# Optimization experiments

Hardware: AMD Instinct MI355X
Metric: run time of the kernel (lower is better)

The kernel has to match this reference:

```python
import jax, jax.numpy as jnp
import numpy as np
import math

B, T, D = 2, 4096, 1024
HD = D // 2                      # head_dim
DEPTH = 12
LAMBDA_INIT = 0.8 - 0.6 * math.exp(-0.3 * DEPTH)
SCALING = HD ** -0.5
EPS = 1e-5


def setup_inputs() -> dict:
    key = jax.random.key(0)
    ks = jax.random.split(key, 11)
    f32 = jnp.float32
    return {
        "q": jax.random.normal(ks[0], (B, T, D), f32),
        "k": jax.random.normal(ks[1], (B, T, D), f32),
        "v": jax.random.normal(ks[2], (B, T, D), f32),
        "Wq": jax.random.normal(ks[3], (D, D), f32) * 0.02,
        "Wk": jax.random.normal(ks[4], (HD, D), f32) * 0.02,
        "Wv": jax.random.normal(ks[5], (D, D), f32) * 0.02,
        "Wo": jax.random.normal(ks[6], (D, D), f32) * 0.02,
        "lambda_q1": jax.random.normal(ks[7], (HD,), f32) * 0.1,
        "lambda_k1": jax.random.normal(ks[8], (HD,), f32) * 0.1,
        "lambda_q2": jax.random.normal(ks[9], (HD,), f32) * 0.1,
        "lambda_k2": jax.random.normal(ks[10], (HD,), f32) * 0.1,
    }


def reference(q, k, v, Wq, Wk, Wv, Wo, lambda_q1, lambda_k1, lambda_q2, lambda_k2):
    b, t, d = q.shape
    s = k.shape[1]
    # projections (Linear with no bias: x @ W.T)
    qp = (q @ Wq.T).reshape(b, t, 2, HD).transpose(0, 2, 1, 3) * SCALING  # [b,2,t,hd]
    kp = k @ Wk.T                                                          # [b,s,hd] (shared by both score heads)
    # dual score maps + softmax over src
    scores = jnp.einsum("bhtd,bsd->bhts", qp, kp)                          # [b,2,t,s]
    scores = jax.nn.softmax(scores.astype(jnp.float32), axis=-1).astype(qp.dtype)
    # lambda-weighted subtraction
    lam1 = jnp.exp(jnp.sum(lambda_q1 * lambda_k1))
    lam2 = jnp.exp(jnp.sum(lambda_q2 * lambda_k2))
    lam = lam1 - lam2 + LAMBDA_INIT
    attn_w = scores[:, 0] - lam * scores[:, 1]                             # [b,t,s]
    # value matmul
    vp = v @ Wv.T                                                          # [b,s,d]
    attn = jnp.einsum("bts,bsd->btd", attn_w, vp)                          # [b,t,d]
    # RMSNorm over last dim (2*head_dim == d), no affine
    rms = jax.lax.rsqrt(jnp.mean(jnp.square(attn), axis=-1, keepdims=True) + EPS)
    attn = attn * rms * (1.0 - LAMBDA_INIT)
    return attn @ Wo.T
```

## Files before the change

kernel.cpp:

```cpp
#include <hip/hip_runtime.h>
#include <stdint.h>
#include <stddef.h>

#define T_   4096
#define BT_  8192
#define SCALING_F      0.04419417382415922f
#define LAMBDA_INIT_F  0.7836057665316212f
#define ONE_MINUS_LI_F 0.2163942334683788f

typedef __attribute__((ext_vector_type(8))) short short8;
typedef __attribute__((ext_vector_type(4))) short short4v;
typedef __attribute__((ext_vector_type(4))) float f32x4;

__device__ __forceinline__ short f2bf(float f){
  uint32_t u = __float_as_uint(f);
  uint32_t r = (u + 0x7fffu + ((u >> 16) & 1u)) >> 16;
  return (short)(uint16_t)r;
}

__device__ __forceinline__ f32x4 mfma16(short8 a, short8 b, f32x4 c){
  return __builtin_amdgcn_mfma_f32_16x16x32_bf16(a, b, c, 0, 0, 0);
}

__device__ __forceinline__ void stage16(short* lds, const short* g){
  __builtin_amdgcn_global_load_lds(
      (const __attribute__((address_space(1))) void*)g,
      (__attribute__((address_space(3))) void*)lds, 16, 0, 0);
}

__global__ void k_cvt(const float* __restrict__ in, short* __restrict__ out, int n4){
  int i  = blockIdx.x*blockDim.x + threadIdx.x;
  int st = gridDim.x*blockDim.x;
  for (; i < n4; i += st){
    float4 v = ((const float4*)in)[i];
    short4v o;
    o.x = f2bf(v.x); o.y = f2bf(v.y); o.z = f2bf(v.z); o.w = f2bf(v.w);
    ((short4v*)out)[i] = o;
  }
}

template<int EPI>
__global__ __launch_bounds__(256, 3) void k_gemm(const short* __restrict__ A,
                                                 const short* __restrict__ Bm,
                                                 void* __restrict__ Cp, int ldc){
  __shared__ short As[128*32];
  __shared__ short Bs[128*32];
  const int tid = threadIdx.x;
  const int w = tid >> 6, l = tid & 63;
  const int m0 = blockIdx.x * 128;
  const int n0 = blockIdx.y * 128;
  const int wr = w >> 1, wc = w & 1;

  f32x4 acc[4][4] = {};

  const short* gA = A  + (size_t)(m0 + w*32 + (l>>2))*1024 + (l&3)*8;
  const short* gB = Bm + (size_t)(n0 + w*32 + (l>>2))*1024 + (l&3)*8;

  for (int k0 = 0; k0 < 1024; k0 += 32){
    stage16(As + w*1024,       gA + k0);
    stage16(As + w*1024 + 512, gA + 16*1024 + k0);
    stage16(Bs + w*1024,       gB + k0);
    stage16(Bs + w*1024 + 512, gB + 16*1024 + k0);
    __syncthreads();
    short8 aF[4], bF[4];
    #pragma unroll
    for (int i = 0; i < 4; i++){
      aF[i] = *(const short8*)&As[(wr*64 + i*16 + (l&15))*32 + (l>>4)*8];
      bF[i] = *(const short8*)&Bs[(wc*64 + i*16 + (l&15))*32 + (l>>4)*8];
    }
    #pragma unroll
    for (int i = 0; i < 4; i++)
      #pragma unroll
      for (int j = 0; j < 4; j++)
        acc[i][j] = mfma16(aF[i], bF[j], acc[i][j]);
    __syncthreads();
  }

  #pragma unroll
  for (int i = 0; i < 4; i++){
    #pragma unroll
    for (int j = 0; j < 4; j++){
      const size_t r0 = (size_t)m0 + wr*64 + i*16 + (l>>4)*4;
      const size_t c  = (size_t)n0 + wc*64 + j*16 + (l&15);
      #pragma unroll
      for (int rg = 0; rg < 4; rg++){
        float v = acc[i][j][rg];
        if (EPI == 2){
          ((float*)Cp)[(r0+rg)*(size_t)ldc + c] = v;
        } else {
          if (EPI == 1) v *= SCALING_F;
          ((short*)Cp)[(r0+rg)*(size_t)ldc + c] = f2bf(v);
        }
      }
    }
  }
}

__global__ __launch_bounds__(512, 2) void k_attn(
    const short* __restrict__ QP, const short* __restrict__ KP,
    const short* __restrict__ VPT,
    const float* __restrict__ lq1, const float* __restrict__ lk1,
    const float* __restrict__ lq2, const float* __restrict__ lk2,
    short* __restrict__ Ab)
{
  __shared__ short Ks[2][64*512];
  __shared__ short Pl[2][32][72];
  __shared__ float lsum[8][16];
  __shared__ float rinv[2][32];
  __shared__ float ssq[8][32];

  int wg = blockIdx.x;
  wg = (wg & 7)*32 + (wg >> 3);
  const int b  = wg >> 7;
  const int t0 = (wg & 127) * 32;

  const int tid = threadIdx.x;
  const int w = tid >> 6, l = tid & 63;

  float s1 = 0.f, s2 = 0.f;
  #pragma unroll
  for (int i = 0; i < 8; i++){
    int idx = l*8 + i;
    s1 += lq1[idx]*lk1[idx];
    s2 += lq2[idx]*lk2[idx];
  }
  #pragma unroll
  for (int off = 1; off < 64; off <<= 1){
    s1 += __shfl_xor(s1, off, 64);
    s2 += __shfl_xor(s2, off, 64);
  }
  const float lam = __expf(s1) - __expf(s2) + LAMBDA_INIT_F;

  const int rc = w >> 1, h = rc >> 1, tch = rc & 1, scb = w & 1;
  short8 qF[16];
  {
    const short* qb = QP + (size_t)(b*T_ + t0 + tch*16 + (l&15))*1024 + h*512 + (l>>4)*8;
    #pragma unroll
    for (int kk = 0; kk < 16; kk++) qF[kk] = *(const short8*)(qb + kk*32);
  }

  f32x4 acc[4][8] = {};
  float lacc[4] = {0.f,0.f,0.f,0.f};

  const short* kpb = KP  + (size_t)(b*T_)*512;
  const short* vb  = VPT + (size_t)(w*128 + (l&15))*BT_ + b*T_ + (l>>4)*8;

  const int jx = (l >> 4) ^ (l & 3);
  const int kx = (l >> 2) & 1;
  const int row0 = (2*scb)*16 + (l & 15);

  {
    short* kdst = &Ks[0][w*8*512];
    const short* ksrc = kpb + (size_t)(w*8)*512;
    #pragma unroll
    for (int j = 0; j < 8; j++)
      stage16(kdst + j*512, ksrc + (size_t)j*512 + ((l ^ j)*8));
  }
  __syncthreads();

  for (int st = 0; st < 64; st++){
    const int s0  = st*64;
    const int cur = st & 1;

    f32x4 sa0 = {0.f,0.f,0.f,0.f}, sa1 = {0.f,0.f,0.f,0.f};
    {
      const short* p0 = &Ks[cur][0] + row0*512 + jx*8;
      const short* p1 = p0 + 16*512;
      #pragma unroll
      for (int kk = 0; kk < 16; kk++){
        short8 b0 = *(const short8*)(p0 + ((kk ^ kx) << 5));
        short8 b1 = *(const short8*)(p1 + ((kk ^ kx) << 5));
        sa0 = mfma16(qF[kk], b0, sa0);
        sa1 = mfma16(qF[kk], b1, sa1);
      }
    }

    if (st + 1 < 64){
      short* kdst = &Ks[cur ^ 1][w*8*512];
      const short* ksrc = kpb + (size_t)((st+1)*64 + w*8)*512;
      #pragma unroll
      for (int j = 0; j < 8; j++)
        stage16(kdst + j*512, ksrc + (size_t)j*512 + ((l ^ j)*8));
    }

    #pragma unroll
    for (int rg = 0; rg < 4; rg++){
      float e0 = __expf(sa0[rg]);
      float e1 = __expf(sa1[rg]);
      lacc[rg] += e0 + e1;
      int row = tch*16 + (l>>4)*4 + rg;
      Pl[h][row][(2*scb+0)*16 + (l&15)] = f2bf(e0);
      Pl[h][row][(2*scb+1)*16 + (l&15)] = f2bf(e1);
    }

    asm volatile("s_waitcnt lgkmcnt(0)" ::: "memory");
    __builtin_amdgcn_s_barrier();

    #pragma unroll
    for (int ks = 0; ks < 2; ks++){
      short8 pa[4];
      #pragma unroll
      for (int rc2 = 0; rc2 < 4; rc2++)
        pa[rc2] = *(const short8*)&Pl[rc2>>1][(rc2&1)*16 + (l&15)][ks*32 + (l>>4)*8];
      #pragma unroll
      for (int dc = 0; dc < 8; dc++){
        short8 bV = *(const short8*)(vb + (size_t)dc*16*BT_ + s0 + ks*32);
        #pragma unroll
        for (int rc2 = 0; rc2 < 4; rc2++)
          acc[rc2][dc] = mfma16(pa[rc2], bV, acc[rc2][dc]);
      }
    }

    __syncthreads();
  }

  #pragma unroll
  for (int off = 1; off < 16; off <<= 1)
    #pragma unroll
    for (int rg = 0; rg < 4; rg++) lacc[rg] += __shfl_xor(lacc[rg], off, 16);
  if ((l & 15) == 0){
    #pragma unroll
    for (int rg = 0; rg < 4; rg++) lsum[w][(l>>4)*4 + rg] = lacc[rg];
  }
  __syncthreads();
  if (tid < 64){
    int hh = tid >> 5, t = tid & 31;
    int rcc = hh*2 + (t >> 4), ric = t & 15;
    rinv[hh][t] = 1.0f / (lsum[rcc*2][ric] + lsum[rcc*2+1][ric]);
  }
  __syncthreads();

  float ps[2][4] = {};
  #pragma unroll
  for (int tc = 0; tc < 2; tc++){
    #pragma unroll
    for (int dc = 0; dc < 8; dc++){
      #pragma unroll
      for (int rg = 0; rg < 4; rg++){
        int t32 = tc*16 + (l>>4)*4 + rg;
        float o = acc[tc][dc][rg]*rinv[0][t32] - lam*acc[2+tc][dc][rg]*rinv[1][t32];
        ps[tc][rg] += o*o;
      }
    }
  }
  #pragma unroll
  for (int tc = 0; tc < 2; tc++)
    #pragma unroll
    for (int off = 1; off < 16; off <<= 1)
      #pragma unroll
      for (int rg = 0; rg < 4; rg++) ps[tc][rg] += __shfl_xor(ps[tc][rg], off, 16);
  if ((l & 15) == 0){
    #pragma unroll
    for (int tc = 0; tc < 2; tc++)
      #pragma unroll
      for (int rg = 0; rg < 4; rg++) ssq[w][tc*16 + (l>>4)*4 + rg] = ps[tc][rg];
  }
  __syncthreads();

  #pragma unroll
  for (int tc = 0; tc < 2; tc++){
    #pragma unroll
    for (int rg = 0; rg < 4; rg++){
      int t32 = tc*16 + (l>>4)*4 + rg;
      float tot = 0.f;
      #pragma unroll
      for (int w8 = 0; w8 < 8; w8++) tot += ssq[w8][t32];
      float scale = rsqrtf(tot*(1.0f/1024.0f) + 1e-5f) * ONE_MINUS_LI_F;
      short* orow = Ab + (size_t)(b*T_ + t0 + t32)*1024 + w*128 + (l&15);
      #pragma unroll
      for (int dc = 0; dc < 8; dc++){
        float o = acc[tc][dc][rg]*rinv[0][t32] - lam*acc[2+tc][dc][rg]*rinv[1][t32];
        orow[dc*16] = f2bf(o*scale);
      }
    }
  }
}

extern "C" void kernel_launch(void* const* d_in, const int* in_sizes, int n_in,
                              void* d_out, int out_size, void* d_ws, size_t ws_size,
                              hipStream_t stream){
  const float* q   = (const float*)d_in[0];
  const float* k   = (const float*)d_in[1];
  const float* v   = (const float*)d_in[2];
  const float* Wq  = (const float*)d_in[3];
  const float* Wk  = (const float*)d_in[4];
  const float* Wv  = (const float*)d_in[5];
  const float* Wo  = (const float*)d_in[6];
  const float* lq1 = (const float*)d_in[7];
  const float* lk1 = (const float*)d_in[8];
  const float* lq2 = (const float*)d_in[9];
  const float* lk2 = (const float*)d_in[10];

  short* ws   = (short*)d_ws;
  short* qb   = ws;
  short* kb   = qb  + (size_t)8192*1024;
  short* vb   = kb  + (size_t)8192*1024;
  short* Wqb  = vb  + (size_t)8192*1024;
  short* Wkb  = Wqb + (size_t)1024*1024;
  short* Wvb  = Wkb + (size_t)512*1024;
  short* Wob  = Wvb + (size_t)1024*1024;
  short* QPb  = Wob + (size_t)1024*1024;
  short* KPb  = QPb + (size_t)8192*1024;
  short* VPTb = KPb + (size_t)8192*512;
  short* Ab   = qb;

  auto cvt = [&](const float* in, short* out, size_t n){
    int n4 = (int)(n/4);
    int grid = (n4 + 255)/256; if (grid > 2048) grid = 2048;
    k_cvt<<<grid, 256, 0, stream>>>(in, out, n4);
  };
  cvt(q,  qb,  (size_t)8192*1024);
  cvt(k,  kb,  (size_t)8192*1024);
  cvt(v,  vb,  (size_t)8192*1024);
  cvt(Wq, Wqb, (size_t)1024*1024);
  cvt(Wk, Wkb, (size_t)512*1024);
  cvt(Wv, Wvb, (size_t)1024*1024);
  cvt(Wo, Wob, (size_t)1024*1024);

  k_gemm<1><<<dim3(64, 8), 256, 0, stream>>>(qb, Wqb, QPb, 1024);
  k_gemm<0><<<dim3(64, 4), 256, 0, stream>>>(kb, Wkb, KPb, 512);
  k_gemm<0><<<dim3(8, 64), 256, 0, stream>>>(Wvb, vb, VPTb, 8192);
  k_attn<<<dim3(256), 512, 0, stream>>>(QPb, KPb, VPTb, lq1, lk1, lq2, lk2, Ab);
  k_gemm<2><<<dim3(64, 8), 256, 0, stream>>>(Ab, Wob, d_out, 1024);
}
```

Before: 559.8 us.

## Stage Q in LDS, single-buffer K, and prefetch V fragments early

Q fragments now live in LDS instead of 16 registers per lane, and the K tile drops from double to single buffering. The next K tile is loaded after the P barrier, overlapping with the PV MFMAs. All V operands for the step are loaded into registers at the top of the loop, so global latency overlaps with the QK^T compute. This frees Q registers but uses 16 short8 registers for V, and adds an LDS read of Q on every step. Single buffering also puts the K reload on the critical path of the next iteration's barrier.

Result: faster. 452.5 us (-19.2%).

```diff
diff --git a/kernel.cpp b/kernel.cpp
--- a/kernel.cpp
+++ b/kernel.cpp
@@ -103,7 +103,8 @@
     const float* __restrict__ lq2, const float* __restrict__ lk2,
     short* __restrict__ Ab)
 {
-  __shared__ short Ks[2][64*512];
+  __shared__ short Ks[64*512];
+  __shared__ short Qs[32*1024];
   __shared__ short Pl[2][32][72];
   __shared__ float lsum[8][16];
   __shared__ float rinv[2][32];
@@ -132,55 +133,56 @@
   const float lam = __expf(s1) - __expf(s2) + LAMBDA_INIT_F;
 
   const int rc = w >> 1, h = rc >> 1, tch = rc & 1, scb = w & 1;
-  short8 qF[16];
-  {
-    const short* qb = QP + (size_t)(b*T_ + t0 + tch*16 + (l&15))*1024 + h*512 + (l>>4)*8;
-    #pragma unroll
-    for (int kk = 0; kk < 16; kk++) qF[kk] = *(const short8*)(qb + kk*32);
-  }
 
   f32x4 acc[4][8] = {};
   float lacc[4] = {0.f,0.f,0.f,0.f};
 
   const short* kpb = KP  + (size_t)(b*T_)*512;
-  const short* vb  = VPT + (size_t)(w*128 + (l&15))*BT_ + b*T_ + (l>>4)*8;
+  const short* vbp = VPT + (size_t)(w*128 + (l&15))*BT_ + (size_t)b*T_ + (l>>4)*8;
 
   const int jx = (l >> 4) ^ (l & 3);
   const int kx = (l >> 2) & 1;
-  const int row0 = (2*scb)*16 + (l & 15);
 
   {
-    short* kdst = &Ks[0][w*8*512];
-    const short* ksrc = kpb + (size_t)(w*8)*512;
+    const short* qsrc = QP + (size_t)(b*T_ + t0)*1024;
+    #pragma unroll
+    for (int j = 0; j < 4; j++){
+      int r = w*4 + j;
+      #pragma unroll
+      for (int h2 = 0; h2 < 2; h2++)
+        stage16(&Qs[r*1024 + h2*512],
+                qsrc + (size_t)r*1024 + (h2*64 + (l ^ (r & 7)))*8);
+    }
     #pragma unroll
     for (int j = 0; j < 8; j++)
-      stage16(kdst + j*512, ksrc + (size_t)j*512 + ((l ^ j)*8));
+      stage16(&Ks[(w*8 + j)*512], kpb + (size_t)(w*8 + j)*512 + ((l ^ j)*8));
   }
   __syncthreads();
 
+  const short* qp0 = &Qs[(tch*16 + (l&15))*1024 + h*512 + jx*8];
+  const short* kp0 = &Ks[(scb*32 + (l&15))*512 + jx*8];
+  const short* kp1 = kp0 + 16*512;
+
   for (int st = 0; st < 64; st++){
-    const int s0  = st*64;
-    const int cur = st & 1;
+    const int s0 = st*64;
+
+    short8 varr[16];
+    #pragma unroll
+    for (int dc = 0; dc < 8; dc++)
+      #pragma unroll
+      for (int ks = 0; ks < 2; ks++)
+        varr[dc*2 + ks] = *(const short8*)(vbp + (size_t)dc*16*BT_ + s0 + ks*32);
+    __builtin_amdgcn_sched_barrier(0);
 
     f32x4 sa0 = {0.f,0.f,0.f,0.f}, sa1 = {0.f,0.f,0.f,0.f};
-    {
-      const short* p0 = &Ks[cur][0] + row0*512 + jx*8;
-      const short* p1 = p0 + 16*512;
-      #pragma unroll
-      for (int kk = 0; kk < 16; kk++){
-        short8 b0 = *(const short8*)(p0 + ((kk ^ kx) << 5));
-        short8 b1 = *(const short8*)(p1 + ((kk ^ kx) << 5));
-        sa0 = mfma16(qF[kk], b0, sa0);
-        sa1 = mfma16(qF[kk], b1, sa1);
-      }
-    }
-
-    if (st + 1 < 64){
-      short* kdst = &Ks[cur ^ 1][w*8*512];
-      const short* ksrc = kpb + (size_t)((st+1)*64 + w*8)*512;
-      #pragma unroll
-      for (int j = 0; j < 8; j++)
-        stage16(kdst + j*512, ksrc + (size_t)j*512 + ((l ^ j)*8));
+    #pragma unroll
+    for (int kk = 0; kk < 16; kk++){
+      const int ko = ((kk ^ kx) << 5);
+      short8 qf = *(const short8*)(qp0 + ko);
+      short8 b0 = *(const short8*)(kp0 + ko);
+      short8 b1 = *(const short8*)(kp1 + ko);
+      sa0 = mfma16(qf, b0, sa0);
+      sa1 = mfma16(qf, b1, sa1);
     }
 
     #pragma unroll
@@ -196,6 +198,13 @@
     asm volatile("s_waitcnt lgkmcnt(0)" ::: "memory");
     __builtin_amdgcn_s_barrier();
 
+    if (st + 1 < 64){
+      const short* ksrc = kpb + (size_t)((st+1)*64 + w*8)*512;
+      #pragma unroll
+      for (int j = 0; j < 8; j++)
+        stage16(&Ks[(w*8 + j)*512], ksrc + (size_t)j*512 + ((l ^ j)*8));
+    }
+
     #pragma unroll
     for (int ks = 0; ks < 2; ks++){
       short8 pa[4];
@@ -203,12 +212,10 @@
       for (int rc2 = 0; rc2 < 4; rc2++)
         pa[rc2] = *(const short8*)&Pl[rc2>>1][(rc2&1)*16 + (l&15)][ks*32 + (l>>4)*8];
       #pragma unroll
-      for (int dc = 0; dc < 8; dc++){
-        short8 bV = *(const short8*)(vb + (size_t)dc*16*BT_ + s0 + ks*32);
+      for (int dc = 0; dc < 8; dc++)
         #pragma unroll
         for (int rc2 = 0; rc2 < 4; rc2++)
-          acc[rc2][dc] = mfma16(pa[rc2], bV, acc[rc2][dc]);
-      }
+          acc[rc2][dc] = mfma16(pa[rc2], varr[dc*2 + ks], acc[rc2][dc]);
     }
 
     __syncthreads();
```

## Reorder attention loop: early K prefetch, hoisted V loads, sched barriers, setprio

Applied to the files above, without the earlier changes.

Moves the next K tile's global-to-LDS staging ahead of the QK^T MFMAs and splits the score loop in half. The V-operand global loads for both 32-wide chunks are issued early into registers, so their latency hides behind the score MFMAs and the softmax barrier. Sched barriers and s_setprio pin the ordering and favour MFMA issue, and the lambda computation moves after the main loop to ease register pressure early on. The cost is more live registers (16 short8 V fragments), which may reduce occupancy or cause spills.

Result: slower. 727.8 us (+30.0%).

```diff
diff --git a/kernel.cpp b/kernel.cpp
--- a/kernel.cpp
+++ b/kernel.cpp
@@ -117,21 +117,17 @@
   const int tid = threadIdx.x;
   const int w = tid >> 6, l = tid & 63;
 
-  float s1 = 0.f, s2 = 0.f;
-  #pragma unroll
-  for (int i = 0; i < 8; i++){
-    int idx = l*8 + i;
-    s1 += lq1[idx]*lk1[idx];
-    s2 += lq2[idx]*lk2[idx];
-  }
-  #pragma unroll
-  for (int off = 1; off < 64; off <<= 1){
-    s1 += __shfl_xor(s1, off, 64);
-    s2 += __shfl_xor(s2, off, 64);
-  }
-  const float lam = __expf(s1) - __expf(s2) + LAMBDA_INIT_F;
-
   const int rc = w >> 1, h = rc >> 1, tch = rc & 1, scb = w & 1;
+
+  f32x4 acc[4][8] = {};
+  float lacc[4] = {0.f,0.f,0.f,0.f};
+
+  const short* kpb = KP  + (size_t)(b*T_)*512;
+  const short* vbp = VPT + (size_t)(w*128 + (l&15))*BT_ + (size_t)b*T_ + (l>>4)*8;
+
+  const int jx = (l >> 4) ^ (l & 3);
+  const int kx = (l >> 2) & 1;
+
   short8 qF[16];
   {
     const short* qb = QP + (size_t)(b*T_ + t0 + tch*16 + (l&15))*1024 + h*512 + (l>>4)*8;
@@ -139,49 +135,54 @@
     for (int kk = 0; kk < 16; kk++) qF[kk] = *(const short8*)(qb + kk*32);
   }
 
-  f32x4 acc[4][8] = {};
-  float lacc[4] = {0.f,0.f,0.f,0.f};
-
-  const short* kpb = KP  + (size_t)(b*T_)*512;
-  const short* vb  = VPT + (size_t)(w*128 + (l&15))*BT_ + b*T_ + (l>>4)*8;
-
-  const int jx = (l >> 4) ^ (l & 3);
-  const int kx = (l >> 2) & 1;
-  const int row0 = (2*scb)*16 + (l & 15);
-
-  {
-    short* kdst = &Ks[0][w*8*512];
-    const short* ksrc = kpb + (size_t)(w*8)*512;
-    #pragma unroll
-    for (int j = 0; j < 8; j++)
-      stage16(kdst + j*512, ksrc + (size_t)j*512 + ((l ^ j)*8));
-  }
+  #pragma unroll
+  for (int j = 0; j < 8; j++)
+    stage16(&Ks[0][(w*8 + j)*512], kpb + (size_t)(w*8 + j)*512 + ((l ^ j)*8));
   __syncthreads();
 
   for (int st = 0; st < 64; st++){
     const int s0  = st*64;
     const int cur = st & 1;
 
+    if (st + 1 < 64){
+      const short* ksrc = kpb + (size_t)((st+1)*64 + w*8)*512;
+      #pragma unroll
+      for (int j = 0; j < 8; j++)
+        stage16(&Ks[cur ^ 1][(w*8 + j)*512], ksrc + (size_t)j*512 + ((l ^ j)*8));
+    }
+    __builtin_amdgcn_sched_barrier(0);
+
+    const short* kp0 = &Ks[cur][(scb*32 + (l&15))*512 + jx*8];
+    const short* kp1 = kp0 + 16*512;
+
     f32x4 sa0 = {0.f,0.f,0.f,0.f}, sa1 = {0.f,0.f,0.f,0.f};
-    {
-      const short* p0 = &Ks[cur][0] + row0*512 + jx*8;
-      const short* p1 = p0 + 16*512;
-      #pragma unroll
-      for (int kk = 0; kk < 16; kk++){
-        short8 b0 = *(const short8*)(p0 + ((kk ^ kx) << 5));
-        short8 b1 = *(const short8*)(p1 + ((kk ^ kx) << 5));
-        sa0 = mfma16(qF[kk], b0, sa0);
-        sa1 = mfma16(qF[kk], b1, sa1);
-      }
-    }
-
-    if (st + 1 < 64){
-      short* kdst = &Ks[cur ^ 1][w*8*512];
-      const short* ksrc = kpb + (size_t)((st+1)*64 + w*8)*512;
-      #pragma unroll
-      for (int j = 0; j < 8; j++)
-        stage16(kdst + j*512, ksrc + (size_t)j*512 + ((l ^ j)*8));
-    }
+    __builtin_amdgcn_s_setprio(1);
+    #pragma unroll
+    for (int kk = 0; kk < 8; kk++){
+      const int ko = ((kk ^ kx) << 5);
+      short8 b0 = *(const short8*)(kp0 + ko);
+      short8 b1 = *(const short8*)(kp1 + ko);
+      sa0 = mfma16(qF[kk], b0, sa0);
+      sa1 = mfma16(qF[kk], b1, sa1);
+    }
+    __builtin_amdgcn_s_setprio(0);
+
+    short8 varr0[8];
+    #pragma unroll
+    for (int dc = 0; dc < 8; dc++)
+      varr0[dc] = *(const short8*)(vbp + (size_t)dc*16*BT_ + s0);
+    __builtin_amdgcn_sched_barrier(0);
+
+    __builtin_amdgcn_s_setprio(1);
+    #pragma unroll
+    for (int kk = 8; kk < 16; kk++){
+      const int ko = ((kk ^ kx) << 5);
+      short8 b0 = *(const short8*)(kp0 + ko);
+      short8 b1 = *(const short8*)(kp1 + ko);
+      sa0 = mfma16(qF[kk], b0, sa0);
+      sa1 = mfma16(qF[kk], b1, sa1);
+    }
+    __builtin_amdgcn_s_setprio(0);
 
     #pragma unroll
     for (int rg = 0; rg < 4; rg++){
@@ -196,23 +197,55 @@
     asm volatile("s_waitcnt lgkmcnt(0)" ::: "memory");
     __builtin_amdgcn_s_barrier();
 
-    #pragma unroll
-    for (int ks = 0; ks < 2; ks++){
+    short8 varr1[8];
+    #pragma unroll
+    for (int dc = 0; dc < 8; dc++)
+      varr1[dc] = *(const short8*)(vbp + (size_t)dc*16*BT_ + s0 + 32);
+    __builtin_amdgcn_sched_barrier(0);
+
+    {
       short8 pa[4];
       #pragma unroll
       for (int rc2 = 0; rc2 < 4; rc2++)
-        pa[rc2] = *(const short8*)&Pl[rc2>>1][(rc2&1)*16 + (l&15)][ks*32 + (l>>4)*8];
-      #pragma unroll
-      for (int dc = 0; dc < 8; dc++){
-        short8 bV = *(const short8*)(vb + (size_t)dc*16*BT_ + s0 + ks*32);
+        pa[rc2] = *(const short8*)&Pl[rc2>>1][(rc2&1)*16 + (l&15)][(l>>4)*8];
+      __builtin_amdgcn_s_setprio(1);
+      #pragma unroll
+      for (int dc = 0; dc < 8; dc++)
         #pragma unroll
         for (int rc2 = 0; rc2 < 4; rc2++)
-          acc[rc2][dc] = mfma16(pa[rc2], bV, acc[rc2][dc]);
-      }
+          acc[rc2][dc] = mfma16(pa[rc2], varr0[dc], acc[rc2][dc]);
+      __builtin_amdgcn_s_setprio(0);
+    }
+    {
+      short8 pa[4];
+      #pragma unroll
+      for (int rc2 = 0; rc2 < 4; rc2++)
+        pa[rc2] = *(const short8*)&Pl[rc2>>1][(rc2&1)*16 + (l&15)][32 + (l>>4)*8];
+      __builtin_amdgcn_s_setprio(1);
+      #pragma unroll
+      for (int dc = 0; dc < 8; dc++)
+        #pragma unroll
+        for (int rc2 = 0; rc2 < 4; rc2++)
+          acc[rc2][dc] = mfma16(pa[rc2], varr1[dc], acc[rc2][dc]);
+      __builtin_amdgcn_s_setprio(0);
     }
 
     __syncthreads();
   }
+
+  float s1 = 0.f, s2 = 0.f;
+  #pragma unroll
+  for (int i = 0; i < 8; i++){
+    int idx = l*8 + i;
+    s1 += lq1[idx]*lk1[idx];
+    s2 += lq2[idx]*lk2[idx];
+  }
+  #pragma unroll
+  for (int off = 1; off < 64; off <<= 1){
+    s1 += __shfl_xor(s1, off, 64);
+    s2 += __shfl_xor(s2, off, 64);
+  }
+  const float lam = __expf(s1) - __expf(s2) + LAMBDA_INIT_F;
 
   #pragma unroll
   for (int off = 1; off < 16; off <<= 1)
```
